# Kernel tuning notes

Hardware: AMD Instinct MI355X
Metric: run time of the kernel (lower is better)

## Reference

```python
import jax, jax.numpy as jnp
import numpy as np

# S4 (liquid-S4, degree=1) forward: diagonal bilinear-discretized SSM kernel,
# FFT global convolution, D skip, liquid correction term, gelu + output linear.

LIQUID_DEGREE = 1


def _forward(u, log_dt, w_re, w_im, B_re, B_im, C_re, C_im, D, W, bias):
    Bb, H, L = u.shape
    dt = jnp.exp(log_dt)                              # (H,)
    w = w_re + 1j * w_im                              # (H, N/2)
    w = jnp.concatenate([w, jnp.conj(w)], axis=-1)    # _conj -> (H, N)
    Bp = B_re + 1j * B_im
    Bp = jnp.concatenate([Bp, jnp.conj(Bp)], axis=-1)  # (H, N)
    Cp = C_re + 1j * C_im
    Cp = jnp.concatenate([Cp, jnp.conj(Cp)], axis=-1)  # (C, H, N)

    denom = 1.0 - 0.5 * dt[:, None] * w               # (H, N)
    dA = (1.0 + 0.5 * dt[:, None] * w) / denom        # bilinear discretization
    dB = dt[:, None] * Bp / denom                     # (H, N), matches diag_embed formula

    # SSM convolution kernel k[c,h,l] = Re( sum_n C[c,h,n] * dB[h,n] * dA[h,n]^l )
    ell = jnp.arange(L)
    V = jnp.exp(jnp.log(dA)[:, :, None] * ell)        # (H, N, L) Vandermonde
    k = jnp.einsum('chn,hn,hnl->chl', Cp, dB, V).real.astype(u.dtype)  # (C, H, L)

    # FFT circular-to-linear convolution (pad to 2L)
    n = 2 * L
    k_f = jnp.fft.rfft(k, n=n)                        # (C, H, L+1)
    u_f = jnp.fft.rfft(u, n=n)                        # (B, H, L+1)
    y = jnp.fft.irfft(u_f[:, None] * k_f[None], n=n)[..., :L]  # (B, C, H, L)
    y = y + u[:, None] * D[None, :, :, None]          # D skip: 'bhl,ch->bchl'

    # Liquid correction terms
    us = u
    dBl = dB
    for _ in range(LIQUID_DEGREE):
        us = us * jnp.pad(us[..., :-1], ((0, 0), (0, 0), (1, 0)))   # u_t * u_{t-1}
        dBl = dBl * jnp.sum(dBl, axis=-1, keepdims=True)            # (dB1*dB2).sum(2)
        dCB = jnp.einsum('chn,hn->ch', Cp, dBl).real                # (C, H) real part (.float())
        y = y + us[:, None] * dCB[None, :, :, None]                 # (B, C, H, L)

    y = y.reshape(Bb, -1, L)                          # (B, C*H, L)
    y = jax.nn.gelu(y)
    y = jnp.einsum('oh,bhl->bol', W, y) + bias[None, :, None]  # output_linear (1x1 conv)
    return y


def setup_inputs() -> dict:
    key = jax.random.key(0)
    ks = jax.random.split(key, 8)
    Bsz, H, L, N2, C = 4, 256, 4096, 32, 1
    u = jax.random.normal(ks[0], (Bsz, H, L), jnp.float32)
    # dt log-uniform in [1e-3, 1e-1] (standard S4 init)
    lo, hi = np.log(1e-3), np.log(1e-1)
    log_dt = (lo + (hi - lo) * jax.random.uniform(ks[1], (H,))).astype(jnp.float32)
    # S4D-Lin style eigenvalues: w = -1/2 + i*pi*n (stable: Re(w) < 0)
    w_re = -0.5 * jnp.ones((H, N2), jnp.float32)
    w_im = jnp.tile(jnp.pi * jnp.arange(N2, dtype=jnp.float32), (H, 1))
    B_re = jax.random.normal(ks[2], (H, N2), jnp.float32)
    B_im = jax.random.normal(ks[3], (H, N2), jnp.float32)
    C_re = jax.random.normal(ks[4], (C, H, N2), jnp.float32) * 0.5
    C_im = jax.random.normal(ks[5], (C, H, N2), jnp.float32) * 0.5
    D = jax.random.normal(ks[6], (C, H), jnp.float32)
    W = jax.random.normal(ks[7], (H, C * H), jnp.float32) / np.sqrt(C * H)
    bias = jnp.zeros((H,), jnp.float32)
    return {"u": u, "log_dt": log_dt, "w_re": w_re, "w_im": w_im,
            "B_re": B_re, "B_im": B_im, "C_re": C_re, "C_im": C_im,
            "D": D, "W": W, "bias": bias}


def reference(u, log_dt, w_re, w_im, B_re, B_im, C_re, C_im, D, W, bias):
    return _forward(u, log_dt, w_re, w_im, B_re, B_im, C_re, C_im, D, W, bias)
```

## Files before the change

### kernel.cpp

```cpp
#include <hip/hip_runtime.h>
#include <math.h>


#define H 256
#define LSEQ 4096
#define NB 4
#define NMODES 32
#define T 64
#define NC 64
#define NSEG 4
#define SEGC 16

typedef _Float16 f16;
typedef _Float16 f16x2 __attribute__((ext_vector_type(2)));
typedef _Float16 f16x4 __attribute__((ext_vector_type(4)));
typedef _Float16 f16x8 __attribute__((ext_vector_type(8)));
typedef float f32x4 __attribute__((ext_vector_type(4)));
union U16x8 { f16x8 v; f16x2 h[4]; uint4 q; };
union U16x4 { f16x4 v; f16x2 h[2]; };

static __device__ __forceinline__ f16x2 pk(float a, float b) {
    typedef __fp16 fp16x2n __attribute__((ext_vector_type(2)));
    fp16x2n r = __builtin_amdgcn_cvt_pkrtz(a, b);
    return __builtin_bit_cast(f16x2, r);
}

__global__ __launch_bounds__(512) void k_setup(
    const float* __restrict__ log_dt, const float* __restrict__ w_re, const float* __restrict__ w_im,
    const float* __restrict__ B_re, const float* __restrict__ B_im,
    const float* __restrict__ C_re, const float* __restrict__ C_im,
    const float* __restrict__ W,
    float2* __restrict__ P, f16* __restrict__ Mh, f16* __restrict__ Wh,
    float2* __restrict__ dAT, float* __restrict__ dCB)
{
    __shared__ float ks_lds[T];
    __shared__ float ERe_lds[NMODES * T];
    __shared__ float EIm_lds[NMODES * T];

    int tid = threadIdx.x;
    int h = blockIdx.x;
    int n = tid & 31;
    int pg = tid >> 5;
    int hn = h * NMODES + n;

    if (tid < 256) Wh[h * 256 + tid] = (f16)W[h * 256 + tid];

    double dt = exp((double)log_dt[h]);
    double zr = 0.5 * dt * (double)w_re[hn], zi = 0.5 * dt * (double)w_im[hn];
    double dr = 1.0 - zr, di = -zi;
    double dn = dr * dr + di * di;
    double nr = 1.0 + zr, ni = zi;
    double dAr = (nr * dr + ni * di) / dn, dAi = (ni * dr - nr * di) / dn;
    double tbr = dt * (double)B_re[hn], tbi = dt * (double)B_im[hn];
    double dBr = (tbr * dr + tbi * di) / dn, dBi = (tbi * dr - tbr * di) / dn;
    double Cr = (double)C_re[hn], Ci = (double)C_im[hn];
    double CBr = Cr * dBr - Ci * dBi, CBi = Cr * dBi + Ci * dBr;

    double d2r = dAr*dAr - dAi*dAi,  d2i = 2.0*dAr*dAi;
    double d4r = d2r*d2r - d2i*d2i,  d4i = 2.0*d2r*d2i;
    double d8r = d4r*d4r - d4i*d4i,  d8i = 2.0*d4r*d4i;
    double d16r= d8r*d8r - d8i*d8i,  d16i= 2.0*d8r*d8i;
    double d32r= d16r*d16r - d16i*d16i, d32i = 2.0*d16r*d16i;
    double ar = 1.0, ai = 0.0;
    if (pg & 1) { double t0 = ar*d4r - ai*d4i;  ai = ar*d4i + ai*d4r;  ar = t0; }
    if (pg & 2) { double t0 = ar*d8r - ai*d8i;  ai = ar*d8i + ai*d8r;  ar = t0; }
    if (pg & 4) { double t0 = ar*d16r - ai*d16i; ai = ar*d16i + ai*d16r; ar = t0; }
    if (pg & 8) { double t0 = ar*d32r - ai*d32i; ai = ar*d32i + ai*d32r; ar = t0; }

    #pragma unroll
    for (int i = 0; i < 4; ++i) {
        int p = pg * 4 + i;
        double pr = dBr * ar - dBi * ai, pi = dBr * ai + dBi * ar;
        P[(h * T + p) * NMODES + n] = make_float2((float)pr, (float)pi);
        float q = (float)(CBr * ar - CBi * ai);
        #pragma unroll
        for (int m = 16; m >= 1; m >>= 1) q += __shfl_xor(q, m);
        if (n == 0) ks_lds[p] = 2.0f * q;
        double nar = ar * dAr - ai * dAi;
        ai = ar * dAi + ai * dAr; ar = nar;
        ERe_lds[n * T + p] = (float)(2.0 * (Cr * ar - Ci * ai));
        EIm_lds[n * T + p] = (float)(2.0 * (Cr * ai + Ci * ar));
    }
    if (pg == 15) dAT[hn] = make_float2((float)ar, (float)ai);
    if (pg == 0) {
        float s1 = (float)dBr, s2 = (float)CBr;
        #pragma unroll
        for (int m = 16; m >= 1; m >>= 1) { s1 += __shfl_xor(s1, m); s2 += __shfl_xor(s2, m); }
        if (n == 0) dCB[h] = 4.0f * s1 * s2;
    }
    __syncthreads();

    int t = tid >> 3, kq = tid & 7;
    U16x8 w4[2];
    #pragma unroll
    for (int i = 0; i < 16; ++i) {
        int k = kq * 16 + i;
        float val;
        if (k < 64)       val = (k <= t) ? ks_lds[t - k] : 0.f;
        else if (k < 96)  val = ERe_lds[(k - 64) * T + t];
        else              val = EIm_lds[(k - 96) * T + t];
        w4[i >> 3].h[(i >> 1) & 3][i & 1] = (f16)val;
    }
    uint4* dst = (uint4*)(Mh + ((size_t)(h * T) + t) * 128 + kq * 16);
    dst[0] = w4[0].q;
    dst[1] = w4[1].q;
}

__global__ __launch_bounds__(256) void k_local(
    const float* __restrict__ u, const float2* __restrict__ P,
    float* __restrict__ SLre, float* __restrict__ SLim)
{
    __shared__ float u_s[64 * 68];
    int tid = threadIdx.x;
    int bh = blockIdx.x;
    int h = bh & (H - 1);

    const float4* uv4 = (const float4*)(u + (size_t)bh * LSEQ);
    #pragma unroll
    for (int it = 0; it < 4; ++it) {
        int f = tid + it * 256;
        int c = f >> 4, j4 = (f & 15) * 4;
        *(float4*)(&u_s[c * 68 + j4]) = uv4[f];
    }
    __syncthreads();

    int n16 = tid & 15, cq = tid >> 4;
    float2 acc[4][2];
    #pragma unroll
    for (int i = 0; i < 4; ++i) { acc[i][0] = make_float2(0.f,0.f); acc[i][1] = make_float2(0.f,0.f); }

    const float4* P4 = (const float4*)P;
    size_t prow = (size_t)h * T;
    #pragma unroll 4
    for (int j = 0; j < T; ++j) {
        float4 pv = P4[(prow + (T - 1 - j)) * 16 + n16];
        #pragma unroll
        for (int i = 0; i < 4; ++i) {
            float uval = u_s[(cq * 4 + i) * 68 + j];
            acc[i][0].x += pv.x * uval; acc[i][0].y += pv.y * uval;
            acc[i][1].x += pv.z * uval; acc[i][1].y += pv.w * uval;
        }
    }
    #pragma unroll
    for (int i = 0; i < 4; ++i) {
        int c = cq * 4 + i;
        size_t idx = ((size_t)bh * NC + c) * NMODES + 2 * n16;
        *(float2*)(SLre + idx) = make_float2(acc[i][0].x, acc[i][1].x);
        *(float2*)(SLim + idx) = make_float2(acc[i][0].y, acc[i][1].y);
    }
}

__global__ __launch_bounds__(256) void k_scanA(
    const float2* __restrict__ dAT, float* __restrict__ SLre, float* __restrict__ SLim,
    float2* __restrict__ Carry)
{
    int gid = blockIdx.x * 256 + threadIdx.x;
    int n = gid & 31;
    int seg = (gid >> 5) & 3;
    int bh = gid >> 7;
    int h = bh & (H - 1);
    float2 A = dAT[h * NMODES + n];
    float Sr = 0.f, Si = 0.f;
    size_t base = ((size_t)bh * NC + seg * SEGC) * NMODES + n;
    for (int r = 0; r < SEGC; ++r) {
        size_t idx = base + (size_t)r * NMODES;
        float lr = SLre[idx], li = SLim[idx];
        SLre[idx] = Sr; SLim[idx] = Si;
        float ns = Sr * A.x - Si * A.y + lr;
        Si = Sr * A.y + Si * A.x + li;
        Sr = ns;
    }
    Carry[((size_t)bh * NSEG + seg) * NMODES + n] = make_float2(Sr, Si);
}

__global__ __launch_bounds__(256) void k_scanB(
    const float2* __restrict__ dAT, float* __restrict__ SLre, float* __restrict__ SLim,
    const float2* __restrict__ Carry)
{
    int gid = blockIdx.x * 256 + threadIdx.x;
    int n = gid & 31;
    int seg = (gid >> 5) & 3;
    int bh = gid >> 7;
    int h = bh & (H - 1);
    float2 A = dAT[h * NMODES + n];
    float ar = A.x, ai = A.y;
    #pragma unroll
    for (int s = 0; s < 4; ++s) { float t = ar*ar - ai*ai; ai = 2.f*ar*ai; ar = t; }
    float Er = 0.f, Ei = 0.f;
    const float2* Cb = Carry + (size_t)bh * NSEG * NMODES + n;
    for (int j = 0; j < seg; ++j) {
        float2 C = Cb[(size_t)j * NMODES];
        float t = Er * ar - Ei * ai + C.x;
        Ei = Er * ai + Ei * ar + C.y;
        Er = t;
    }
    float Vr = Er, Vi = Ei;
    size_t base = ((size_t)bh * NC + seg * SEGC) * NMODES + n;
    for (int r = 0; r < SEGC; ++r) {
        size_t idx = base + (size_t)r * NMODES;
        float lr = SLre[idx], li = SLim[idx];
        SLre[idx] = Vr + lr;
        SLim[idx] = -(Vi + li);
        float t = Vr * A.x - Vi * A.y;
        Vi = Vr * A.y + Vi * A.x;
        Vr = t;
    }
}

__global__ __launch_bounds__(256) void k_main(
    const float* __restrict__ u, const f16* __restrict__ Mh,
    const float* __restrict__ SLre, const float* __restrict__ SLim,
    const float* __restrict__ dCB, const float* __restrict__ D,
    f16* __restrict__ YG)
{
    int h = blockIdx.x;
    int qq = blockIdx.y;
    int tid = threadIdx.x;
    int w = tid >> 6, lane = tid & 63;
    int l15 = lane & 15, g = lane >> 4;

    int q = qq * 64 + w * 16 + l15;
    int b = q >> 6, c = q & 63;

    f32x4 acc[4];
    #pragma unroll
    for (int i = 0; i < 4; ++i) acc[i] = (f32x4)0.f;

    const f16* Mbase = Mh + (size_t)h * T * 128;

    #pragma unroll
    for (int s = 0; s < 4; ++s) {
        f16x8 a4[4];
        #pragma unroll
        for (int tt = 0; tt < 4; ++tt)
            a4[tt] = *(const f16x8*)(Mbase + (tt * 16 + l15) * 128 + 32 * s + 8 * g);

        U16x8 bf;
        f32x4 lo, hi;
        if (s < 2) {
            int j0 = 32 * s + 8 * g;
            const float* up = u + ((size_t)(b * H + h)) * LSEQ + c * T + j0;
            lo = *(const f32x4*)up;
            hi = *(const f32x4*)(up + 4);
        } else {
            int n0 = 8 * g;
            const float* sp = (s == 2 ? SLre : SLim) +
                              ((size_t)(b * H + h) * NC + c) * NMODES + n0;
            lo = *(const f32x4*)sp;
            hi = *(const f32x4*)(sp + 4);
        }
        bf.h[0] = pk(lo.x, lo.y);
        bf.h[1] = pk(lo.z, lo.w);
        bf.h[2] = pk(hi.x, hi.y);
        bf.h[3] = pk(hi.z, hi.w);
        #pragma unroll
        for (int tt = 0; tt < 4; ++tt)
            acc[tt] = __builtin_amdgcn_mfma_f32_16x16x32_f16(a4[tt], bf.v, acc[tt], 0, 0, 0);
    }

    float Dh = D[h], dCBh = dCB[h];
    #pragma unroll
    for (int tt = 0; tt < 4; ++tt) {
        int l0 = c * T + tt * 16 + g * 4;
        const float* ub = u + ((size_t)(b * H + h)) * LSEQ;
        f32x4 uv = *(const f32x4*)(ub + l0);
        float up0 = (l0 == 0) ? 0.f : ub[l0 - 1];
        float ups[4] = {up0, uv.x, uv.y, uv.z};
        f32x4 out4;
        #pragma unroll
        for (int r = 0; r < 4; ++r) {
            float y = acc[tt][r] + Dh * uv[r] + dCBh * uv[r] * ups[r];
            float y3 = y * y * y;
            out4[r] = 0.5f * y * (1.f + tanhf(0.7978845608028654f * (y + 0.044715f * y3)));
        }
        U16x4 o16;
        o16.h[0] = pk(out4[0], out4[1]);
        o16.h[1] = pk(out4[2], out4[3]);
        *(f16x4*)(YG + ((size_t)(b * H + h)) * LSEQ + l0) = o16.v;
    }
}

#define KO_STRIDE 40
__global__ __launch_bounds__(256) void k_out(
    const f16* __restrict__ YG, const f16* __restrict__ Wh,
    const float* __restrict__ bias, float* __restrict__ out)
{
    __shared__ f16 lds_b[32 * KO_STRIDE];
    int tid = threadIdx.x;
    int w = tid >> 6, lane = tid & 63;
    int l15 = lane & 15, g = lane >> 4;
    int Lb = blockIdx.x * 32;
    int b = Lb >> 12, lbase = Lb & 4095;
    int o0 = w * 64;

    int hh = tid >> 3, l4 = (tid & 7) * 4;

    f32x4 acc[4][2];
    #pragma unroll
    for (int i = 0; i < 4; ++i) { acc[i][0] = (f32x4)0.f; acc[i][1] = (f32x4)0.f; }

    const f16* ygb = YG + ((size_t)(b * H + hh)) * LSEQ + lbase + l4;
    f16x4 v = *(const f16x4*)ygb;

    for (int k = 0; k < 8; ++k) {
        if (k) __syncthreads();
        #pragma unroll
        for (int i = 0; i < 4; ++i) lds_b[(l4 + i) * KO_STRIDE + hh] = v[i];
        if (k < 7) v = *(const f16x4*)(ygb + (size_t)(k + 1) * 32 * LSEQ);
        __syncthreads();

        f16x8 bf[2];
        #pragma unroll
        for (int lt = 0; lt < 2; ++lt)
            bf[lt] = *(const f16x8*)(&lds_b[(lt * 16 + l15) * KO_STRIDE + 8 * g]);
        #pragma unroll
        for (int ot = 0; ot < 4; ++ot) {
            f16x8 a = *(const f16x8*)(Wh + (size_t)(o0 + ot * 16 + l15) * 256 + k * 32 + 8 * g);
            acc[ot][0] = __builtin_amdgcn_mfma_f32_16x16x32_f16(a, bf[0], acc[ot][0], 0, 0, 0);
            acc[ot][1] = __builtin_amdgcn_mfma_f32_16x16x32_f16(a, bf[1], acc[ot][1], 0, 0, 0);
        }
    }

    #pragma unroll
    for (int ot = 0; ot < 4; ++ot) {
        #pragma unroll
        for (int lt = 0; lt < 2; ++lt) {
            int l = lbase + lt * 16 + l15;
            #pragma unroll
            for (int r = 0; r < 4; ++r) {
                int o = o0 + ot * 16 + g * 4 + r;
                out[((size_t)(b * 256 + o)) * LSEQ + l] = acc[ot][lt][r] + bias[o];
            }
        }
    }
}

extern "C" void kernel_launch(void* const* d_in, const int* in_sizes, int n_in,
                              void* d_out, int out_size, void* d_ws, size_t ws_size,
                              hipStream_t stream) {
    const float* u      = (const float*)d_in[0];
    const float* log_dt = (const float*)d_in[1];
    const float* w_re   = (const float*)d_in[2];
    const float* w_im   = (const float*)d_in[3];
    const float* B_re   = (const float*)d_in[4];
    const float* B_im   = (const float*)d_in[5];
    const float* C_re   = (const float*)d_in[6];
    const float* C_im   = (const float*)d_in[7];
    const float* Dp     = (const float*)d_in[8];
    const float* Wp     = (const float*)d_in[9];
    const float* bias   = (const float*)d_in[10];
    float* out = (float*)d_out;
    float* ws = (float*)d_ws;

    float2* P    = (float2*)(ws);
    f16*    Mh   = (f16*)(ws + 1048576);
    f16*    Wh   = (f16*)(ws + 2097152);
    float2* dAT  = (float2*)(ws + 2129920);
    float*  dCB  = ws + 2146304;
    float*  SLre = ws + 2146560;
    float*  SLim = ws + 4243712;
    f16*    YG16 = (f16*)(ws + 6340864);
    float2* Carry = (float2*)(ws);

    k_setup<<<H, 512, 0, stream>>>(log_dt, w_re, w_im, B_re, B_im, C_re, C_im,
                                   Wp, P, Mh, Wh, dAT, dCB);
    k_local<<<NB * H, 256, 0, stream>>>(u, P, SLre, SLim);
    k_scanA<<<NB * H * NSEG * NMODES / 256, 256, 0, stream>>>(dAT, SLre, SLim, Carry);
    k_scanB<<<NB * H * NSEG * NMODES / 256, 256, 0, stream>>>(dAT, SLre, SLim, Carry);
    dim3 gm(H, 4);
    k_main<<<gm, 256, 0, stream>>>(u, Mh, SLre, SLim, dCB, Dp, YG16);
    k_out<<<NB * LSEQ / 32, 256, 0, stream>>>(YG16, Wh, bias, out);
}
```

Baseline: 146.3 us.

## Fuse chunk-state scan into local projection kernel via in-block LDS scan

Removes the two separate scan kernels (segmented scan plus carry propagation) and performs the inter-chunk state recurrence inside the local projection kernel. Each thread combines its 4 chunks, totals are shared through LDS, and each thread serially prefixes earlier groups using dA^4 powers before writing exclusive states. This eliminates two kernel launches and the global read/write round trips of SLre/SLim and the Carry buffer, at the cost of a serial loop of up to 15 steps per thread and an extra barrier.

```diff
diff --git a/kernel.cpp b/kernel.cpp
--- a/kernel.cpp
+++ b/kernel.cpp
@@ -8,8 +8,6 @@
 #define NMODES 32
 #define T 64
 #define NC 64
-#define NSEG 4
-#define SEGC 16
 
 typedef _Float16 f16;
 typedef _Float16 f16x2 __attribute__((ext_vector_type(2)));
@@ -23,6 +21,10 @@
     typedef __fp16 fp16x2n __attribute__((ext_vector_type(2)));
     fp16x2n r = __builtin_amdgcn_cvt_pkrtz(a, b);
     return __builtin_bit_cast(f16x2, r);
+}
+
+static __device__ __forceinline__ float2 cmul(float2 a, float2 b) {
+    return make_float2(a.x * b.x - a.y * b.y, a.x * b.y + a.y * b.x);
 }
 
 __global__ __launch_bounds__(512) void k_setup(
@@ -106,11 +108,13 @@
     dst[1] = w4[1].q;
 }
 
-__global__ __launch_bounds__(256) void k_local(
+__global__ __launch_bounds__(256) void k_lscan(
     const float* __restrict__ u, const float2* __restrict__ P,
+    const float2* __restrict__ dAT,
     float* __restrict__ SLre, float* __restrict__ SLim)
 {
     __shared__ float u_s[64 * 68];
+    __shared__ float4 tot_lds[16][16];
     int tid = threadIdx.x;
     int bh = blockIdx.x;
     int h = bh & (H - 1);
@@ -141,69 +145,36 @@
             acc[i][1].x += pv.z * uval; acc[i][1].y += pv.w * uval;
         }
     }
+
+    float2 A0 = dAT[h * NMODES + 2 * n16];
+    float2 A1 = dAT[h * NMODES + 2 * n16 + 1];
+
+    float2 T0 = make_float2(0.f, 0.f), T1 = make_float2(0.f, 0.f);
+    #pragma unroll
+    for (int i = 0; i < 4; ++i) {
+        T0 = cmul(A0, T0); T0.x += acc[i][0].x; T0.y += acc[i][0].y;
+        T1 = cmul(A1, T1); T1.x += acc[i][1].x; T1.y += acc[i][1].y;
+    }
+    tot_lds[cq][n16] = make_float4(T0.x, T0.y, T1.x, T1.y);
+    __syncthreads();
+
+    float2 R0 = cmul(A0, A0); R0 = cmul(R0, R0);
+    float2 R1 = cmul(A1, A1); R1 = cmul(R1, R1);
+    float2 S0 = make_float2(0.f, 0.f), S1 = make_float2(0.f, 0.f);
+    for (int j = 0; j < cq; ++j) {
+        float4 t = tot_lds[j][n16];
+        S0 = cmul(R0, S0); S0.x += t.x; S0.y += t.y;
+        S1 = cmul(R1, S1); S1.x += t.z; S1.y += t.w;
+    }
+
     #pragma unroll
     for (int i = 0; i < 4; ++i) {
         int c = cq * 4 + i;
         size_t idx = ((size_t)bh * NC + c) * NMODES + 2 * n16;
-        *(float2*)(SLre + idx) = make_float2(acc[i][0].x, acc[i][1].x);
-        *(float2*)(SLim + idx) = make_float2(acc[i][0].y, acc[i][1].y);
-    }
-}
-
-__global__ __launch_bounds__(256) void k_scanA(
-    const float2* __restrict__ dAT, float* __restrict__ SLre, float* __restrict__ SLim,
-    float2* __restrict__ Carry)
-{
-    int gid = blockIdx.x * 256 + threadIdx.x;
-    int n = gid & 31;
-    int seg = (gid >> 5) & 3;
-    int bh = gid >> 7;
-    int h = bh & (H - 1);
-    float2 A = dAT[h * NMODES + n];
-    float Sr = 0.f, Si = 0.f;
-    size_t base = ((size_t)bh * NC + seg * SEGC) * NMODES + n;
-    for (int r = 0; r < SEGC; ++r) {
-        size_t idx = base + (size_t)r * NMODES;
-        float lr = SLre[idx], li = SLim[idx];
-        SLre[idx] = Sr; SLim[idx] = Si;
-        float ns = Sr * A.x - Si * A.y + lr;
-        Si = Sr * A.y + Si * A.x + li;
-        Sr = ns;
-    }
-    Carry[((size_t)bh * NSEG + seg) * NMODES + n] = make_float2(Sr, Si);
-}
-
-__global__ __launch_bounds__(256) void k_scanB(
-    const float2* __restrict__ dAT, float* __restrict__ SLre, float* __restrict__ SLim,
-    const float2* __restrict__ Carry)
-{
-    int gid = blockIdx.x * 256 + threadIdx.x;
-    int n = gid & 31;
-    int seg = (gid >> 5) & 3;
-    int bh = gid >> 7;
-    int h = bh & (H - 1);
-    float2 A = dAT[h * NMODES + n];
-    float ar = A.x, ai = A.y;
-    #pragma unroll
-    for (int s = 0; s < 4; ++s) { float t = ar*ar - ai*ai; ai = 2.f*ar*ai; ar = t; }
-    float Er = 0.f, Ei = 0.f;
-    const float2* Cb = Carry + (size_t)bh * NSEG * NMODES + n;
-    for (int j = 0; j < seg; ++j) {
-        float2 C = Cb[(size_t)j * NMODES];
-        float t = Er * ar - Ei * ai + C.x;
-        Ei = Er * ai + Ei * ar + C.y;
-        Er = t;
-    }
-    float Vr = Er, Vi = Ei;
-    size_t base = ((size_t)bh * NC + seg * SEGC) * NMODES + n;
-    for (int r = 0; r < SEGC; ++r) {
-        size_t idx = base + (size_t)r * NMODES;
-        float lr = SLre[idx], li = SLim[idx];
-        SLre[idx] = Vr + lr;
-        SLim[idx] = -(Vi + li);
-        float t = Vr * A.x - Vi * A.y;
-        Vi = Vr * A.y + Vi * A.x;
-        Vr = t;
+        *(float2*)(SLre + idx) = make_float2(S0.x, S1.x);
+        *(float2*)(SLim + idx) = make_float2(-S0.y, -S1.y);
+        S0 = cmul(A0, S0); S0.x += acc[i][0].x; S0.y += acc[i][0].y;
+        S1 = cmul(A1, S1); S1.x += acc[i][1].x; S1.y += acc[i][1].y;
     }
 }
 
@@ -360,13 +331,10 @@
     float*  SLre = ws + 2146560;
     float*  SLim = ws + 4243712;
     f16*    YG16 = (f16*)(ws + 6340864);
-    float2* Carry = (float2*)(ws);
 
     k_setup<<<H, 512, 0, stream>>>(log_dt, w_re, w_im, B_re, B_im, C_re, C_im,
                                    Wp, P, Mh, Wh, dAT, dCB);
-    k_local<<<NB * H, 256, 0, stream>>>(u, P, SLre, SLim);
-    k_scanA<<<NB * H * NSEG * NMODES / 256, 256, 0, stream>>>(dAT, SLre, SLim, Carry);
-    k_scanB<<<NB * H * NSEG * NMODES / 256, 256, 0, stream>>>(dAT, SLre, SLim, Carry);
+    k_lscan<<<NB * H, 256, 0, stream>>>(u, P, dAT, SLre, SLim);
     dim3 gm(H, 4);
     k_main<<<gm, 256, 0, stream>>>(u, Mh, SLre, SLim, dCB, Dp, YG16);
     k_out<<<NB * LSEQ / 32, 256, 0, stream>>>(YG16, Wh, bias, out);
```

Measured after the change: 136.0 us. 7.0% less time.
